# Kernel tuning notes

Measured on AMD Instinct MI355X. Metric: run time of the kernel, lower is better.

Reference implementation:

```python
import jax, jax.numpy as jnp
import numpy as np

OUTPUT_BUDGET = 2048
PADDING_IDX = 0
BIG = 1e9
B, TG, M = 4, 32768, 4
N_ENT, N_REL, D = 100000, 512, 128
N_RULES = 64


def setup_inputs() -> dict:
    key = jax.random.key(0)
    ks = jax.random.split(key, 8)
    # entity ids in [1, N_ENT) so padding_idx=0 is reserved
    subj = jax.random.randint(ks[0], (B, TG, M), 1, N_ENT)
    pred = jax.random.randint(ks[1], (B, TG, M), 0, N_REL)
    obj = jax.random.randint(ks[2], (B, TG, M), 1, N_ENT)
    body = jnp.stack([subj, pred, obj], axis=-1)  # [B, TG, M, 3]
    pad = jax.random.uniform(ks[3], (B, TG, M)) < 0.25
    body = body.at[..., 0].set(jnp.where(pad, PADDING_IDX, body[..., 0]))
    mask = jax.random.uniform(ks[4], (B, TG)) < 0.9  # [B, TG] bool
    rule_idx = jax.random.randint(ks[5], (B, TG), 0, N_RULES)
    ent_emb = jax.random.normal(ks[6], (N_ENT, D), dtype=jnp.float32) * 0.1
    rel_emb = jax.random.normal(ks[7], (N_REL, D), dtype=jnp.float32) * 0.1
    return {"body": body, "mask": mask, "rule_idx": rule_idx,
            "ent_emb": ent_emb, "rel_emb": rel_emb}


def reference(body, mask, rule_idx, ent_emb, rel_emb):
    # KGE (DistMult) atom scoring: gather embeddings, tri-linear dot per atom
    s = ent_emb[body[..., 0]]   # [B, TG, M, D]
    r = rel_emb[body[..., 1]]   # [B, TG, M, D]
    o = ent_emb[body[..., 2]]   # [B, TG, M, D]
    atom_scores = jnp.einsum('btmd,btmd,btmd->btm', s, r, o)  # [B, TG, M]
    body_active = body[..., 0] != PADDING_IDX
    atom_scores = jnp.where(body_active, atom_scores, BIG)
    # min-conjunction over atoms, mask inactive groundings
    scores = jnp.min(atom_scores, axis=-1)            # [B, TG]
    scores = jnp.where(mask, scores, -BIG)
    # top-k select per batch row
    top_scores, top_idx = jax.lax.top_k(scores, OUTPUT_BUDGET)  # [B, K]
    body_sel = jnp.take_along_axis(body, top_idx[:, :, None, None], axis=1)  # [B, K, M, 3]
    mask_sel = jnp.take_along_axis(mask, top_idx, axis=1)        # [B, K]
    rule_sel = jnp.take_along_axis(rule_idx, top_idx, axis=1)    # [B, K]
    return body_sel, mask_sel, rule_sel, top_scores
```

## Files before the change

### kernel.cpp

```cpp
#include <hip/hip_runtime.h>
#include <hip/hip_bf16.h>
#include <hip/hip_fp16.h>
#include <stdint.h>

constexpr int B_    = 4;
constexpr int TG_   = 32768;
constexpr int D_    = 128;
constexpr int KOUT_ = 2048;
constexpr int NH_   = 4096;
constexpr int CAPL_ = 8192;
constexpr long ENTQ_ = 100000L * D_ / 4;
constexpr long RELQ_ = 512L * D_ / 4;
#define BIGF 1e9f

#define WS_KEYS(ws)  ((unsigned long long*)(ws))
#define WS_GHIST(ws) ((uint32_t*)((char*)(ws) + (1u << 20)))
#define WS_REL8(ws)  ((unsigned char*)((char*)(ws) + (2u << 20)))
#define WS_ENT8(ws)  ((unsigned char*)((char*)(ws) + (2u << 20) + 65536u))

__device__ __forceinline__ uint32_t f2u_asc(float f) {
  uint32_t b = __float_as_uint(f);
  return (b & 0x80000000u) ? ~b : (b | 0x80000000u);
}
__device__ __forceinline__ float u2f_asc(uint32_t u) {
  uint32_t b = (u & 0x80000000u) ? (u & 0x7FFFFFFFu) : ~u;
  return __uint_as_float(b);
}

__device__ __forceinline__ bool mask_is_i32(const void* mask_raw) {
  const uint32_t* mw = (const uint32_t*)mask_raw;
  bool i32 = true;
  #pragma unroll
  for (int j = 0; j < 16; ++j) i32 &= (mw[j] <= 1u);
  return i32;
}
__device__ __forceinline__ int read_mask(const void* mask_raw, int idx, bool i32) {
  return i32 ? ((const int*)mask_raw)[idx]
             : (int)((const unsigned char*)mask_raw)[idx];
}

__device__ __forceinline__ uint32_t f2e5m2(float x) {
  uint32_t u = (uint32_t)__half_as_ushort(__float2half(x));
  return (u + 0x7Fu + ((u >> 8) & 1u)) >> 8;
}

__global__ __launch_bounds__(256) void convert_kernel(
    const float* __restrict__ ent, const float* __restrict__ rel,
    unsigned char* __restrict__ ent8, unsigned char* __restrict__ rel8) {
  long stride = (long)gridDim.x * 256;
  for (long q = (long)blockIdx.x * 256 + threadIdx.x; q < ENTQ_ + RELQ_; q += stride) {
    bool isEnt = (q < ENTQ_);
    long qq = isEnt ? q : (q - ENTQ_);
    float4 v = isEnt ? ((const float4*)ent)[qq] : ((const float4*)rel)[qq];
    uint32_t b = f2e5m2(v.x) | (f2e5m2(v.y) << 8) | (f2e5m2(v.z) << 16) | (f2e5m2(v.w) << 24);
    if (isEnt) ((uint32_t*)ent8)[qq] = b;
    else       ((uint32_t*)rel8)[qq] = b;
  }
}

__device__ __forceinline__ void expand4(uint32_t w, uint32_t& lo, uint32_t& hi) {
  lo = ((w << 8) & 0xFF00u)  | ((w << 16) & 0xFF000000u);
  hi = ((w >> 8) & 0xFF00u)  | (w & 0xFF000000u);
}

__device__ __forceinline__ float dot8_e5(uint32_t sx, uint32_t sy,
                                         uint32_t rx, uint32_t ry,
                                         uint32_t ox, uint32_t oy) {
  uint32_t sw[4], rw[4], ow[4];
  expand4(sx, sw[0], sw[1]); expand4(sy, sw[2], sw[3]);
  expand4(rx, rw[0], rw[1]); expand4(ry, rw[2], rw[3]);
  expand4(ox, ow[0], ow[1]); expand4(oy, ow[2], ow[3]);
  const __half2* sh = (const __half2*)sw;
  const __half2* rh = (const __half2*)rw;
  const __half2* oh = (const __half2*)ow;
  __half2 acc = __half2{__ushort_as_half(0), __ushort_as_half(0)};
  #pragma unroll
  for (int c = 0; c < 4; ++c)
    acc = __hfma2(__hmul2(sh[c], rh[c]), oh[c], acc);
  return __low2float(acc) + __high2float(acc);
}

__device__ __forceinline__ float dot16_e5(const uint4& s, const uint4& r, const uint4& o) {
  return dot8_e5(s.x, s.y, r.x, r.y, o.x, o.y)
       + dot8_e5(s.z, s.w, r.z, r.w, o.z, o.w);
}

__global__ __launch_bounds__(256, 4) void score_e5m2_kernel(
    const int* __restrict__ body, const void* __restrict__ mask,
    const unsigned char* __restrict__ ent8, const unsigned char* __restrict__ rel8,
    unsigned long long* __restrict__ keys, uint32_t* __restrict__ ghist) {
  if (blockIdx.x < 64) ghist[blockIdx.x * 256 + threadIdx.x] = 0;
  int lane = threadIdx.x & 63;
  int wv   = threadIdx.x >> 6;
  int wid0 = blockIdx.x * 32 + wv * 8;
  int g    = lane >> 3;
  int sl   = lane & 7;
  int wid  = wid0 + g;
  const uint4* bq = (const uint4*)(body + (long)wid * 12);
  uint4 b0 = bq[0], b1 = bq[1], b2 = bq[2];
  int sI[4] = {(int)b0.x, (int)b0.w, (int)b1.z, (int)b2.y};
  int rI[4] = {(int)b0.y, (int)b1.x, (int)b1.w, (int)b2.z};
  int oI[4] = {(int)b0.z, (int)b1.y, (int)b2.x, (int)b2.w};
  bool pd[4];
  #pragma unroll
  for (int a = 0; a < 4; ++a) {
    pd[a] = (sI[a] == 0);
    if (pd[a]) { rI[a] = 0; oI[a] = 0; }
  }
  uint4 S[4], R[4], O[4];
  #pragma unroll
  for (int a = 0; a < 4; ++a) {
    S[a] = ((const uint4*)(ent8 + (long)sI[a] * D_))[sl];
    R[a] = ((const uint4*)(rel8 + (long)rI[a] * D_))[sl];
    O[a] = ((const uint4*)(ent8 + (long)oI[a] * D_))[sl];
  }
  float q[4];
  #pragma unroll
  for (int a = 0; a < 4; ++a) q[a] = dot16_e5(S[a], R[a], O[a]);
  #pragma unroll
  for (int a = 0; a < 4; ++a) {
    q[a] += __shfl_xor(q[a], 1);
    q[a] += __shfl_xor(q[a], 2);
    q[a] += __shfl_xor(q[a], 4);
    q[a] = pd[a] ? BIGF : q[a];
  }
  float m = fminf(fminf(q[0], q[1]), fminf(q[2], q[3]));
  float sc = read_mask(mask, wid, mask_is_i32(mask)) ? m : -BIGF;
  if (sl == 0) {
    uint32_t dk = ~f2u_asc(sc);
    keys[wid] = ((unsigned long long)dk << 32) | (uint32_t)(wid & (TG_ - 1));
  }
}

__global__ __launch_bounds__(1024) void hist_kernel(
    const unsigned long long* __restrict__ keys, uint32_t* __restrict__ ghist) {
  __shared__ uint32_t lh[NH_];
  int row   = blockIdx.x >> 4;
  int chunk = blockIdx.x & 15;
  int tid = threadIdx.x;
  #pragma unroll
  for (int i = 0; i < NH_ / 1024; ++i) lh[tid + i * 1024] = 0;
  __syncthreads();
  const unsigned long long* kk = keys + (long)row * TG_ + chunk * 2048;
  #pragma unroll
  for (int u = 0; u < 2; ++u)
    atomicAdd(&lh[(uint32_t)(kk[u * 1024 + tid] >> 52)], 1u);
  __syncthreads();
  uint32_t* gh = ghist + row * NH_;
  #pragma unroll
  for (int i = 0; i < NH_ / 1024; ++i) {
    uint32_t v = lh[tid + i * 1024];
    if (v) atomicAdd(&gh[tid + i * 1024], v);
  }
}

__global__ __launch_bounds__(1024) void finish_kernel(
    const unsigned long long* __restrict__ keys, const uint32_t* __restrict__ ghist,
    const int* __restrict__ body, const void* __restrict__ mask,
    const int* __restrict__ rule, float* __restrict__ out) {
  __shared__ uint32_t ofs[NH_];
  __shared__ uint32_t bofs[NH_];
  __shared__ unsigned long long cand[CAPL_];
  __shared__ uint32_t wexc[16];
  __shared__ uint32_t s_th;
  int tid  = threadIdx.x;
  int lane = tid & 63;
  int wv   = tid >> 6;
  int b    = blockIdx.x;
  const unsigned long long* kk = keys + (long)b * TG_;
  const uint32_t* gh = ghist + b * NH_;
  uint4 cq = ((const uint4*)gh)[tid];
  uint32_t c0 = cq.x, c1 = cq.y, c2 = cq.z, c3 = cq.w;
  #pragma unroll
  for (int i = 0; i < NH_ / 1024; ++i) bofs[tid + i * 1024] = 0;
  uint32_t s = c0 + c1 + c2 + c3;
  uint32_t inc = s;
  #pragma unroll
  for (int off = 1; off < 64; off <<= 1) {
    uint32_t t = __shfl_up(inc, off, 64);
    if (lane >= off) inc += t;
  }
  if (lane == 63) wexc[wv] = inc;
  __syncthreads();
  if (tid < 16) {
    uint32_t v = wexc[tid];
    uint32_t iv = v;
    #pragma unroll
    for (int off = 1; off < 16; off <<= 1) {
      uint32_t t = __shfl_up(iv, off, 64);
      if (tid >= off) iv += t;
    }
    wexc[tid] = iv - v;
  }
  __syncthreads();
  uint32_t excl = wexc[wv] + inc - s;
  uint32_t e0 = excl, e1 = e0 + c0, e2 = e1 + c1, e3 = e2 + c2, incl = e3 + c3;
  if (excl < (uint32_t)KOUT_ && incl >= (uint32_t)KOUT_) {
    uint32_t t4 = (uint32_t)tid * 4;
    s_th = (e1 >= (uint32_t)KOUT_) ? t4
         : (e2 >= (uint32_t)KOUT_) ? t4 + 1
         : (e3 >= (uint32_t)KOUT_) ? t4 + 2 : t4 + 3;
  }
  ofs[4*tid] = e0; ofs[4*tid+1] = e1; ofs[4*tid+2] = e2; ofs[4*tid+3] = e3;
  __syncthreads();
  uint32_t th = s_th;
  const uint4* kq = (const uint4*)kk;
  #pragma unroll
  for (int bt = 0; bt < 4; ++bt) {
    int base = (bt * 1024 + tid) * 4;
    uint4 v0 = kq[base], v1 = kq[base+1], v2 = kq[base+2], v3 = kq[base+3];
    uint32_t hi[8] = {v0.y, v0.w, v1.y, v1.w, v2.y, v2.w, v3.y, v3.w};
    uint32_t lo[8] = {v0.x, v0.z, v1.x, v1.z, v2.x, v2.z, v3.x, v3.z};
    #pragma unroll
    for (int j = 0; j < 8; ++j) {
      uint32_t pfx = hi[j] >> 20;
      if (pfx <= th) {
        uint32_t pos = ofs[pfx] + atomicAdd(&bofs[pfx], 1u);
        if (pos < (uint32_t)CAPL_)
          cand[pos] = ((unsigned long long)hi[j] << 32) | lo[j];
      }
    }
  }
  __syncthreads();
  uint32_t n = (th + 1 < (uint32_t)NH_) ? ofs[th + 1] : (uint32_t)TG_;
  if (n > (uint32_t)CAPL_) n = CAPL_;
  bool mi32 = mask_is_i32(mask);
  for (uint32_t slot = tid; slot < n; slot += 1024) {
    unsigned long long my = cand[slot];
    uint32_t pfx = (uint32_t)(my >> 52);
    uint32_t s0 = ofs[pfx];
    uint32_t s1 = (pfx + 1 < (uint32_t)NH_) ? ofs[pfx + 1] : n;
    if (s1 > n) s1 = n;
    uint32_t r = s0;
    for (uint32_t i = s0; i < s1; ++i) r += (cand[i] < my);
    if (r >= (uint32_t)KOUT_) continue;
    int t = (int)(my & 0xFFFFFFFFu);
    float sc = u2f_asc(~(uint32_t)(my >> 32));
    int g = b * TG_ + t;
    int idx = b * KOUT_ + (int)r;
    const int* at = body + (long)g * 12;
    float* ob = out + (long)idx * 12;
    #pragma unroll
    for (int c = 0; c < 12; ++c) ob[c] = (float)at[c];
    const int base1 = B_ * KOUT_ * 12;
    out[base1 + idx]                  = read_mask(mask, g, mi32) ? 1.0f : 0.0f;
    out[base1 + B_ * KOUT_ + idx]     = (float)rule[g];
    out[base1 + 2 * B_ * KOUT_ + idx] = sc;
  }
}

extern "C" void kernel_launch(void* const* d_in, const int* in_sizes, int n_in,
                              void* d_out, int out_size, void* d_ws, size_t ws_size,
                              hipStream_t stream) {
  const int*  body = (const int*)d_in[0];
  const void* mask = d_in[1];
  const int*  rule = (const int*)d_in[2];
  const float* ent = (const float*)d_in[3];
  const float* rel = (const float*)d_in[4];
  float* out = (float*)d_out;

  unsigned long long* keys = WS_KEYS(d_ws);
  uint32_t* ghist = WS_GHIST(d_ws);
  unsigned char* ent8 = WS_ENT8(d_ws);
  unsigned char* rel8 = WS_REL8(d_ws);

  convert_kernel<<<2048, 256, 0, stream>>>(ent, rel, ent8, rel8);
  score_e5m2_kernel<<<(B_ * TG_) / 32, 256, 0, stream>>>(body, mask, ent8, rel8, keys, ghist);
  hist_kernel<<<B_ * 16, 1024, 0, stream>>>(keys, ghist);
  finish_kernel<<<B_, 1024, 0, stream>>>(keys, ghist, body, mask, rule, out);
}
```

Before: 68.96 us.

## Fuse histogram pass into finish kernel and count sentinel keys with registers

Removes the separate histogram kernel and global histogram buffer. The finish kernel now builds the per-row prefix histogram itself in shared memory. Keys equal to the +BIG and -BIG sentinels are counted in registers and wave-reduced, so heavily populated buckets do not suffer shared atomic contention. This drops one launch and the global atomics. In exchange, only 4 blocks now read all keys twice, where 64 blocks did that pass before, so parallelism drops.

```diff
diff --git a/kernel.cpp b/kernel.cpp
--- a/kernel.cpp
+++ b/kernel.cpp
@@ -14,7 +14,6 @@
 #define BIGF 1e9f
 
 #define WS_KEYS(ws)  ((unsigned long long*)(ws))
-#define WS_GHIST(ws) ((uint32_t*)((char*)(ws) + (1u << 20)))
 #define WS_REL8(ws)  ((unsigned char*)((char*)(ws) + (2u << 20)))
 #define WS_ENT8(ws)  ((unsigned char*)((char*)(ws) + (2u << 20) + 65536u))
 
@@ -88,8 +87,7 @@
 __global__ __launch_bounds__(256, 4) void score_e5m2_kernel(
     const int* __restrict__ body, const void* __restrict__ mask,
     const unsigned char* __restrict__ ent8, const unsigned char* __restrict__ rel8,
-    unsigned long long* __restrict__ keys, uint32_t* __restrict__ ghist) {
-  if (blockIdx.x < 64) ghist[blockIdx.x * 256 + threadIdx.x] = 0;
+    unsigned long long* __restrict__ keys) {
   int lane = threadIdx.x & 63;
   int wv   = threadIdx.x >> 6;
   int wid0 = blockIdx.x * 32 + wv * 8;
@@ -132,32 +130,11 @@
   }
 }
 
-__global__ __launch_bounds__(1024) void hist_kernel(
-    const unsigned long long* __restrict__ keys, uint32_t* __restrict__ ghist) {
-  __shared__ uint32_t lh[NH_];
-  int row   = blockIdx.x >> 4;
-  int chunk = blockIdx.x & 15;
-  int tid = threadIdx.x;
-  #pragma unroll
-  for (int i = 0; i < NH_ / 1024; ++i) lh[tid + i * 1024] = 0;
-  __syncthreads();
-  const unsigned long long* kk = keys + (long)row * TG_ + chunk * 2048;
-  #pragma unroll
-  for (int u = 0; u < 2; ++u)
-    atomicAdd(&lh[(uint32_t)(kk[u * 1024 + tid] >> 52)], 1u);
-  __syncthreads();
-  uint32_t* gh = ghist + row * NH_;
-  #pragma unroll
-  for (int i = 0; i < NH_ / 1024; ++i) {
-    uint32_t v = lh[tid + i * 1024];
-    if (v) atomicAdd(&gh[tid + i * 1024], v);
-  }
-}
-
 __global__ __launch_bounds__(1024) void finish_kernel(
-    const unsigned long long* __restrict__ keys, const uint32_t* __restrict__ ghist,
+    const unsigned long long* __restrict__ keys,
     const int* __restrict__ body, const void* __restrict__ mask,
     const int* __restrict__ rule, float* __restrict__ out) {
+  __shared__ uint32_t lh[NH_];
   __shared__ uint32_t ofs[NH_];
   __shared__ uint32_t bofs[NH_];
   __shared__ unsigned long long cand[CAPL_];
@@ -167,12 +144,41 @@
   int lane = tid & 63;
   int wv   = tid >> 6;
   int b    = blockIdx.x;
+  const uint32_t DKP = ~f2u_asc(BIGF);
+  const uint32_t DKN = ~f2u_asc(-BIGF);
   const unsigned long long* kk = keys + (long)b * TG_;
-  const uint32_t* gh = ghist + b * NH_;
-  uint4 cq = ((const uint4*)gh)[tid];
-  uint32_t c0 = cq.x, c1 = cq.y, c2 = cq.z, c3 = cq.w;
-  #pragma unroll
-  for (int i = 0; i < NH_ / 1024; ++i) bofs[tid + i * 1024] = 0;
+  const uint4* kq = (const uint4*)kk;
+  #pragma unroll
+  for (int i = 0; i < NH_ / 1024; ++i) {
+    lh[tid + i * 1024] = 0;
+    bofs[tid + i * 1024] = 0;
+  }
+  __syncthreads();
+  uint32_t pc = 0, nc = 0;
+  #pragma unroll
+  for (int bt = 0; bt < 4; ++bt) {
+    int base = (bt * 1024 + tid) * 4;
+    uint4 v0 = kq[base], v1 = kq[base+1], v2 = kq[base+2], v3 = kq[base+3];
+    uint32_t hi[8] = {v0.y, v0.w, v1.y, v1.w, v2.y, v2.w, v3.y, v3.w};
+    #pragma unroll
+    for (int j = 0; j < 8; ++j) {
+      uint32_t h = hi[j];
+      if (h == DKP)      ++pc;
+      else if (h == DKN) ++nc;
+      else atomicAdd(&lh[h >> 20], 1u);
+    }
+  }
+  #pragma unroll
+  for (int off = 1; off < 64; off <<= 1) {
+    pc += __shfl_xor(pc, off, 64);
+    nc += __shfl_xor(nc, off, 64);
+  }
+  if (lane == 0) {
+    if (pc) atomicAdd(&lh[DKP >> 20], pc);
+    if (nc) atomicAdd(&lh[DKN >> 20], nc);
+  }
+  __syncthreads();
+  uint32_t c0 = lh[4*tid], c1 = lh[4*tid+1], c2 = lh[4*tid+2], c3 = lh[4*tid+3];
   uint32_t s = c0 + c1 + c2 + c3;
   uint32_t inc = s;
   #pragma unroll
@@ -204,7 +210,6 @@
   ofs[4*tid] = e0; ofs[4*tid+1] = e1; ofs[4*tid+2] = e2; ofs[4*tid+3] = e3;
   __syncthreads();
   uint32_t th = s_th;
-  const uint4* kq = (const uint4*)kk;
   #pragma unroll
   for (int bt = 0; bt < 4; ++bt) {
     int base = (bt * 1024 + tid) * 4;
@@ -260,12 +265,10 @@
   float* out = (float*)d_out;
 
   unsigned long long* keys = WS_KEYS(d_ws);
-  uint32_t* ghist = WS_GHIST(d_ws);
   unsigned char* ent8 = WS_ENT8(d_ws);
   unsigned char* rel8 = WS_REL8(d_ws);
 
   convert_kernel<<<2048, 256, 0, stream>>>(ent, rel, ent8, rel8);
-  score_e5m2_kernel<<<(B_ * TG_) / 32, 256, 0, stream>>>(body, mask, ent8, rel8, keys, ghist);
-  hist_kernel<<<B_ * 16, 1024, 0, stream>>>(keys, ghist);
-  finish_kernel<<<B_, 1024, 0, stream>>>(keys, ghist, body, mask, rule, out);
-}
+  score_e5m2_kernel<<<(B_ * TG_) / 32, 256, 0, stream>>>(body, mask, ent8, rel8, keys);
+  finish_kernel<<<B_, 1024, 0, stream>>>(keys, body, mask, rule, out);
+}
```

Result: slower. 92.42 us (+34.0%).

## Pre-sort key chunks by prefix in histogram kernel so finish reads only candidates

Applied to the files above, without the earlier changes.

The histogram kernel now also does a local counting sort of each 2048-key chunk by the 12-bit prefix. It writes the sorted chunk and a per-chunk prefix scan to workspace. The single-block-per-row finish kernel then reads only the leading candidates of each chunk up to the threshold, instead of scanning all 32768 keys per row. This moves serial work from 4 blocks to 64 parallel blocks, at the cost of an extra write and read of the keys plus the scan array.

```diff
diff --git a/kernel.cpp b/kernel.cpp
--- a/kernel.cpp
+++ b/kernel.cpp
@@ -13,10 +13,12 @@
 constexpr long RELQ_ = 512L * D_ / 4;
 #define BIGF 1e9f
 
-#define WS_KEYS(ws)  ((unsigned long long*)(ws))
-#define WS_GHIST(ws) ((uint32_t*)((char*)(ws) + (1u << 20)))
-#define WS_REL8(ws)  ((unsigned char*)((char*)(ws) + (2u << 20)))
-#define WS_ENT8(ws)  ((unsigned char*)((char*)(ws) + (2u << 20) + 65536u))
+#define WS_KEYS(ws)   ((unsigned long long*)(ws))
+#define WS_KEYS2(ws)  ((unsigned long long*)((char*)(ws) + (1u << 20)))
+#define WS_GHIST(ws)  ((uint32_t*)((char*)(ws) + (2u << 20)))
+#define WS_CHSCAN(ws) ((unsigned short*)((char*)(ws) + (2u << 20) + 65536u))
+#define WS_REL8(ws)   ((unsigned char*)((char*)(ws) + (3u << 20)))
+#define WS_ENT8(ws)   ((unsigned char*)((char*)(ws) + (3u << 20) + 65536u))
 
 __device__ __forceinline__ uint32_t f2u_asc(float f) {
   uint32_t b = __float_as_uint(f);
@@ -132,19 +134,23 @@
   }
 }
 
-__global__ __launch_bounds__(1024) void hist_kernel(
-    const unsigned long long* __restrict__ keys, uint32_t* __restrict__ ghist) {
+__global__ __launch_bounds__(1024) void histsort_kernel(
+    const unsigned long long* __restrict__ keys, uint32_t* __restrict__ ghist,
+    unsigned short* __restrict__ chscan, unsigned long long* __restrict__ keys2) {
   __shared__ uint32_t lh[NH_];
+  __shared__ uint32_t lb[NH_];
+  __shared__ unsigned long long srt[2048];
+  __shared__ uint32_t wexc[16];
   int row   = blockIdx.x >> 4;
   int chunk = blockIdx.x & 15;
-  int tid = threadIdx.x;
-  #pragma unroll
-  for (int i = 0; i < NH_ / 1024; ++i) lh[tid + i * 1024] = 0;
-  __syncthreads();
+  int tid = threadIdx.x, lane = tid & 63, wv = tid >> 6;
   const unsigned long long* kk = keys + (long)row * TG_ + chunk * 2048;
   #pragma unroll
-  for (int u = 0; u < 2; ++u)
-    atomicAdd(&lh[(uint32_t)(kk[u * 1024 + tid] >> 52)], 1u);
+  for (int i = 0; i < NH_ / 1024; ++i) { lh[tid + i*1024] = 0; lb[tid + i*1024] = 0; }
+  __syncthreads();
+  unsigned long long k0 = kk[tid], k1 = kk[tid + 1024];
+  atomicAdd(&lh[(uint32_t)(k0 >> 52)], 1u);
+  atomicAdd(&lh[(uint32_t)(k1 >> 52)], 1u);
   __syncthreads();
   uint32_t* gh = ghist + row * NH_;
   #pragma unroll
@@ -152,10 +158,46 @@
     uint32_t v = lh[tid + i * 1024];
     if (v) atomicAdd(&gh[tid + i * 1024], v);
   }
+  uint32_t c0 = lh[4*tid], c1 = lh[4*tid+1], c2 = lh[4*tid+2], c3 = lh[4*tid+3];
+  uint32_t s = c0 + c1 + c2 + c3;
+  uint32_t inc = s;
+  #pragma unroll
+  for (int off = 1; off < 64; off <<= 1) {
+    uint32_t t = __shfl_up(inc, off, 64);
+    if (lane >= off) inc += t;
+  }
+  if (lane == 63) wexc[wv] = inc;
+  __syncthreads();
+  if (tid < 16) {
+    uint32_t v = wexc[tid], iv = v;
+    #pragma unroll
+    for (int off = 1; off < 16; off <<= 1) {
+      uint32_t t = __shfl_up(iv, off, 64);
+      if (tid >= off) iv += t;
+    }
+    wexc[tid] = iv - v;
+  }
+  __syncthreads();
+  uint32_t excl = wexc[wv] + inc - s;
+  uint32_t e0 = excl, e1 = e0 + c0, e2 = e1 + c1, e3 = e2 + c2, incl = e3 + c3;
+  unsigned short* gc = chscan + ((long)row * 16 + chunk) * NH_;
+  ushort4 sv; sv.x = (unsigned short)e1; sv.y = (unsigned short)e2;
+  sv.z = (unsigned short)e3; sv.w = (unsigned short)incl;
+  ((ushort4*)gc)[tid] = sv;
+  lh[4*tid] = e0; lh[4*tid+1] = e1; lh[4*tid+2] = e2; lh[4*tid+3] = e3;
+  __syncthreads();
+  uint32_t p0 = lh[(uint32_t)(k0 >> 52)] + atomicAdd(&lb[(uint32_t)(k0 >> 52)], 1u);
+  srt[p0] = k0;
+  uint32_t p1 = lh[(uint32_t)(k1 >> 52)] + atomicAdd(&lb[(uint32_t)(k1 >> 52)], 1u);
+  srt[p1] = k1;
+  __syncthreads();
+  unsigned long long* k2 = keys2 + ((long)row * 16 + chunk) * 2048;
+  ((uint4*)k2)[tid] = ((const uint4*)srt)[tid];
 }
 
 __global__ __launch_bounds__(1024) void finish_kernel(
-    const unsigned long long* __restrict__ keys, const uint32_t* __restrict__ ghist,
+    const unsigned long long* __restrict__ keys2, const uint32_t* __restrict__ ghist,
+    const unsigned short* __restrict__ chscan,
     const int* __restrict__ body, const void* __restrict__ mask,
     const int* __restrict__ rule, float* __restrict__ out) {
   __shared__ uint32_t ofs[NH_];
@@ -167,7 +209,6 @@
   int lane = tid & 63;
   int wv   = tid >> 6;
   int b    = blockIdx.x;
-  const unsigned long long* kk = keys + (long)b * TG_;
   const uint32_t* gh = ghist + b * NH_;
   uint4 cq = ((const uint4*)gh)[tid];
   uint32_t c0 = cq.x, c1 = cq.y, c2 = cq.z, c3 = cq.w;
@@ -183,8 +224,7 @@
   if (lane == 63) wexc[wv] = inc;
   __syncthreads();
   if (tid < 16) {
-    uint32_t v = wexc[tid];
-    uint32_t iv = v;
+    uint32_t v = wexc[tid], iv = v;
     #pragma unroll
     for (int off = 1; off < 16; off <<= 1) {
       uint32_t t = __shfl_up(iv, off, 64);
@@ -204,22 +244,13 @@
   ofs[4*tid] = e0; ofs[4*tid+1] = e1; ofs[4*tid+2] = e2; ofs[4*tid+3] = e3;
   __syncthreads();
   uint32_t th = s_th;
-  const uint4* kq = (const uint4*)kk;
-  #pragma unroll
-  for (int bt = 0; bt < 4; ++bt) {
-    int base = (bt * 1024 + tid) * 4;
-    uint4 v0 = kq[base], v1 = kq[base+1], v2 = kq[base+2], v3 = kq[base+3];
-    uint32_t hi[8] = {v0.y, v0.w, v1.y, v1.w, v2.y, v2.w, v3.y, v3.w};
-    uint32_t lo[8] = {v0.x, v0.z, v1.x, v1.z, v2.x, v2.z, v3.x, v3.z};
-    #pragma unroll
-    for (int j = 0; j < 8; ++j) {
-      uint32_t pfx = hi[j] >> 20;
-      if (pfx <= th) {
-        uint32_t pos = ofs[pfx] + atomicAdd(&bofs[pfx], 1u);
-        if (pos < (uint32_t)CAPL_)
-          cand[pos] = ((unsigned long long)hi[j] << 32) | lo[j];
-      }
-    }
+  uint32_t cnt = (uint32_t)chscan[((long)b * 16 + wv) * NH_ + th];
+  const unsigned long long* k2 = keys2 + ((long)b * 16 + wv) * 2048;
+  for (uint32_t i = lane; i < cnt; i += 64) {
+    unsigned long long key = k2[i];
+    uint32_t pfx = (uint32_t)(key >> 52);
+    uint32_t pos = ofs[pfx] + atomicAdd(&bofs[pfx], 1u);
+    if (pos < (uint32_t)CAPL_) cand[pos] = key;
   }
   __syncthreads();
   uint32_t n = (th + 1 < (uint32_t)NH_) ? ofs[th + 1] : (uint32_t)TG_;
@@ -259,13 +290,15 @@
   const float* rel = (const float*)d_in[4];
   float* out = (float*)d_out;
 
-  unsigned long long* keys = WS_KEYS(d_ws);
-  uint32_t* ghist = WS_GHIST(d_ws);
-  unsigned char* ent8 = WS_ENT8(d_ws);
-  unsigned char* rel8 = WS_REL8(d_ws);
+  unsigned long long* keys  = WS_KEYS(d_ws);
+  unsigned long long* keys2 = WS_KEYS2(d_ws);
+  uint32_t*       ghist  = WS_GHIST(d_ws);
+  unsigned short* chscan = WS_CHSCAN(d_ws);
+  unsigned char*  ent8   = WS_ENT8(d_ws);
+  unsigned char*  rel8   = WS_REL8(d_ws);
 
   convert_kernel<<<2048, 256, 0, stream>>>(ent, rel, ent8, rel8);
   score_e5m2_kernel<<<(B_ * TG_) / 32, 256, 0, stream>>>(body, mask, ent8, rel8, keys, ghist);
-  hist_kernel<<<B_ * 16, 1024, 0, stream>>>(keys, ghist);
-  finish_kernel<<<B_, 1024, 0, stream>>>(keys, ghist, body, mask, rule, out);
-}
+  histsort_kernel<<<B_ * 16, 1024, 0, stream>>>(keys, ghist, chscan, keys2);
+  finish_kernel<<<B_, 1024, 0, stream>>>(keys2, ghist, chscan, body, mask, rule, out);
+}
```

Measured after the change: 66.91 us, median of 2. -3.0%, faster.
